# Optimization experiments

Hardware: AMD Instinct MI355X
Metric: run time of the kernel (lower is better)

The kernel has to match this reference:

```python
import jax, jax.numpy as jnp
import numpy as np

BN_EPS = 1e-5
W_SCALE = 0.05  # keep pre-softmax logits in a sane range with random weights


def setup_inputs() -> dict:
    key = jax.random.key(0)
    ks = jax.random.split(key, 8)
    b, C, H, W = 2, 512, 80, 80
    Ck, Cv, Co = 256, 256, 512
    return {
        "x": jax.random.normal(ks[0], (b, C, H, W), dtype=jnp.float32),
        "wk": jax.random.normal(ks[1], (Ck, C), dtype=jnp.float32) * W_SCALE,
        "bk": jax.random.normal(ks[2], (Ck,), dtype=jnp.float32) * W_SCALE,
        "gamma": jnp.ones((Ck,), dtype=jnp.float32),
        "beta": jnp.zeros((Ck,), dtype=jnp.float32),
        "rmean": jnp.zeros((Ck,), dtype=jnp.float32),
        "rvar": jnp.ones((Ck,), dtype=jnp.float32),
        "wv": jax.random.normal(ks[3], (Cv, C), dtype=jnp.float32) * W_SCALE,
        "bv": jax.random.normal(ks[4], (Cv,), dtype=jnp.float32) * W_SCALE,
        "wW": jax.random.normal(ks[5], (Co, Cv), dtype=jnp.float32) * W_SCALE,
        "bW": jax.random.normal(ks[6], (Co,), dtype=jnp.float32) * W_SCALE,
    }


def reference(x, wk, bk, gamma, beta, rmean, rvar, wv, bv, wW, bW):
    b, C, H, Wd = x.shape
    N = H * Wd
    Ck = wk.shape[0]
    Cv = wv.shape[0]
    # f_key == f_query (shared module): 1x1 conv + BN(inference) + ReLU
    k = jnp.einsum('bchw,oc->bohw', x, wk) + bk[:, None, None]
    scale_bn = gamma / jnp.sqrt(rvar + BN_EPS)
    k = (k - rmean[:, None, None]) * scale_bn[:, None, None] + beta[:, None, None]
    k = jax.nn.relu(k).reshape(b, Ck, N)          # [b, Ck, N]
    q = jnp.transpose(k, (0, 2, 1))               # [b, N, Ck] (query shares weights with key)
    # f_value: plain 1x1 conv
    v = (jnp.einsum('bchw,oc->bohw', x, wv) + bv[:, None, None]).reshape(b, Cv, N)
    sim = jnp.einsum('bnc,bcm->bnm', q, k) * (Ck ** -0.5)  # [b, N, N]
    sim = jax.nn.softmax(sim, axis=-1)
    ctx = jnp.einsum('bnm,bvm->bvn', sim, v).reshape(b, Cv, H, Wd)
    out = jnp.einsum('bvhw,ov->bohw', ctx, wW) + bW[:, None, None]
    return out
```

## Files before the change

kernel.cpp:

```cpp
#include <hip/hip_runtime.h>
#include <stdint.h>

typedef __attribute__((ext_vector_type(8))) short bf16x8;
typedef __attribute__((ext_vector_type(4))) float f32x4;

__device__ __forceinline__ ushort f2bf(float f) {
    union { float f; uint32_t i; } v; v.f = f;
    uint32_t r = v.i + 0x7fff + ((v.i >> 16) & 1);
    return (ushort)(r >> 16);
}
__device__ __forceinline__ uint32_t cvtpk(float lo, float hi) {
    uint32_t r;
    asm("v_cvt_pk_bf16_f32 %0, %1, %2" : "=v"(r) : "v"(lo), "v"(hi));
    return r;
}

typedef unsigned int uint_as1 __attribute__((address_space(1)));
typedef unsigned int uint_as3 __attribute__((address_space(3)));
__device__ __forceinline__ void async16(const void* g, void* l) {
    __builtin_amdgcn_global_load_lds((const uint_as1*)g, (uint_as3*)l, 16, 0, 0);
}

__global__ void prep_all(const float* __restrict__ wk, const float* __restrict__ wv,
                         const float* __restrict__ wW,
                         const float* __restrict__ bk, const float* __restrict__ gamma,
                         const float* __restrict__ beta, const float* __restrict__ rmean,
                         const float* __restrict__ rvar,
                         ushort* __restrict__ wkb, ushort* __restrict__ wvb,
                         ushort* __restrict__ wWb,
                         float* __restrict__ scaleA, float* __restrict__ shiftA) {
    const int b = blockIdx.x;
    if (b == 1536) {
        int i = threadIdx.x;
        float s = gamma[i] * rsqrtf(rvar[i] + 1e-5f);
        scaleA[i] = 0.25f * s;
        shiftA[i] = 0.25f * ((bk[i] - rmean[i]) * s + beta[i]);
        return;
    }
    const int i = (b & 511) * 256 + threadIdx.x;
    const float* src = (b < 512) ? wk : (b < 1024) ? wv : wW;
    ushort* dst = (b < 512) ? wkb : (b < 1024) ? wvb : wWb;
    dst[i] = f2bf(src[i]);
}

__global__ void transpose_cvt(const float* __restrict__ x, ushort* __restrict__ xt) {
    __shared__ float t[32][33];
    int b = blockIdx.z;
    int n0 = blockIdx.x * 32, c0 = blockIdx.y * 32;
    const float* xb = x + (size_t)b * 512 * 6400;
    ushort* xtb = xt + (size_t)b * 6400 * 512;
    int tx = threadIdx.x, ty = threadIdx.y;
    t[ty][tx] = xb[(size_t)(c0 + ty) * 6400 + n0 + tx];
    __syncthreads();
    xtb[(size_t)(n0 + ty) * 512 + c0 + tx] = f2bf(t[tx][ty]);
}

template <int EPI>
__device__ __forceinline__ void gemm_body(
    int bxi, int byi, int bzi,
    const ushort* __restrict__ A, const ushort* __restrict__ B, void* __restrict__ Cout,
    int K, int lda, int ldb, int ldc,
    size_t zsa, size_t zsb, size_t zsc,
    const float* __restrict__ vec0, const float* __restrict__ vec1,
    float* __restrict__ rsum, ushort* smem) {

    A += (size_t)bzi * zsa;
    B += (size_t)bzi * zsb;

    const int tid = threadIdx.x;
    const int lane = tid & 63, wave = tid >> 6;
    const int wm = wave & 1, wn = wave >> 1;
    const int bM = byi * 128, bN = bxi * 128;

    const int sr = lane >> 2;
    const int scs = ((lane & 3) ^ ((lane >> 3) & 3)) * 8;
    const ushort* gA0 = A + (size_t)(bM + wave * 32 + sr) * lda + scs;
    const ushort* gA1 = gA0 + (size_t)16 * lda;
    const ushort* gB0 = B + (size_t)(bN + wave * 32 + sr) * ldb + scs;
    const ushort* gB1 = gB0 + (size_t)16 * ldb;
    ushort* lAw = &smem[wave * 1024];
    ushort* lBw = &smem[3 * 4096 + wave * 1024];

    const int rowA = wm * 64;
    const int rowB = wn * 64;
    const int fr = lane & 15;
    const int fk = ((lane >> 4) ^ ((fr >> 1) & 3)) * 8;

    f32x4 acc[4][4] = {};
    const int nT = K >> 5;

    auto stage = [&](int t, int buf) {
        const int k0 = t * 32;
        const int ob = buf * 4096;
        async16(gA0 + k0, lAw + ob);
        async16(gA1 + k0, lAw + ob + 512);
        async16(gB0 + k0, lBw + ob);
        async16(gB1 + k0, lBw + ob + 512);
    };

    stage(0, 0);
    if (nT > 1) stage(1, 1);

    for (int t = 0; t < nT; ++t) {
        if (t + 1 < nT) { asm volatile("s_waitcnt vmcnt(4)" ::: "memory"); }
        else            { asm volatile("s_waitcnt vmcnt(0)" ::: "memory"); }
        __builtin_amdgcn_sched_barrier(0);
        __builtin_amdgcn_s_barrier();
        __builtin_amdgcn_sched_barrier(0);
        if (t + 2 < nT) stage(t + 2, (t + 2) % 3);
        const int cur = t % 3;
        const ushort* lA = &smem[cur * 4096];
        const ushort* lB = &smem[3 * 4096 + cur * 4096];
        bf16x8 af[4], bff[4];
#pragma unroll
        for (int mi = 0; mi < 4; mi++)
            af[mi] = *(const bf16x8*)&lA[(rowA + mi * 16 + fr) * 32 + fk];
#pragma unroll
        for (int ni = 0; ni < 4; ni++)
            bff[ni] = *(const bf16x8*)&lB[(rowB + ni * 16 + fr) * 32 + fk];
#pragma unroll
        for (int mi = 0; mi < 4; mi++)
#pragma unroll
            for (int ni = 0; ni < 4; ni++)
                acc[mi][ni] = __builtin_amdgcn_mfma_f32_16x16x32_bf16(af[mi], bff[ni], acc[mi][ni], 0, 0, 0);
        __builtin_amdgcn_sched_barrier(0);
    }
    __builtin_amdgcn_s_barrier();
    __builtin_amdgcn_sched_barrier(0);

    float* Cf = (float*)Cout + (size_t)bzi * zsc;
    ushort* Cu = (ushort*)Cout + (size_t)bzi * zsc;
    float* lt = (float*)smem;
    const int g4 = (lane >> 4) * 4;
    const int cl = lane & 15;
    const int lr = tid >> 3;
    const int ch = tid & 7;

    if (EPI == 6) {
        const bool diag = (bxi == byi);
        float creg[16];
#pragma unroll
        for (int i = 0; i < 16; i++) creg[i] = 0.f;
#pragma unroll
        for (int mi = 0; mi < 4; ++mi) {
#pragma unroll
            for (int ni = 0; ni < 4; ++ni) {
                const int lcol = wn * 64 + ni * 16 + cl;
#pragma unroll
                for (int r = 0; r < 4; ++r)
                    lt[(wm * 16 + g4 + r) * 132 + lcol] = acc[mi][ni][r];
            }
            __syncthreads();
            const int brow = (lr < 16) ? (mi * 16 + lr) : (64 + mi * 16 + (lr - 16));
            const int grow = bM + brow;
            const int gcol = bN + ch * 16;
            float vv[16];
#pragma unroll
            for (int i = 0; i < 16; i += 4) {
                f32x4 q = *(const f32x4*)&lt[lr * 132 + ch * 16 + i];
                vv[i] = __expf(q[0]); vv[i + 1] = __expf(q[1]);
                vv[i + 2] = __expf(q[2]); vv[i + 3] = __expf(q[3]);
            }
            float ssum = 0.f;
#pragma unroll
            for (int i = 0; i < 16; i++) { ssum += vv[i]; creg[i] += vv[i]; }
            ssum += __shfl_down(ssum, 4, 8);
            ssum += __shfl_down(ssum, 2, 8);
            ssum += __shfl_down(ssum, 1, 8);
            if (ch == 0) rsum[(size_t)bxi * 6400 + grow] = ssum;
            uint4 q0 = { cvtpk(vv[0], vv[1]), cvtpk(vv[2], vv[3]),
                         cvtpk(vv[4], vv[5]), cvtpk(vv[6], vv[7]) };
            uint4 q1 = { cvtpk(vv[8], vv[9]), cvtpk(vv[10], vv[11]),
                         cvtpk(vv[12], vv[13]), cvtpk(vv[14], vv[15]) };
            *(uint4*)&Cu[(size_t)grow * ldc + gcol] = q0;
            *(uint4*)&Cu[(size_t)grow * ldc + gcol + 8] = q1;
            if (!diag) {
#pragma unroll
                for (int i = 0; i < 16; i++) lt[lr * 132 + ch * 16 + i] = vv[i];
                __syncthreads();
                const int j = tid >> 1, h = tid & 1;
                ushort mo[16];
#pragma unroll
                for (int i = 0; i < 16; i += 2) {
                    float a = lt[(h * 16 + i) * 132 + j];
                    float b2 = lt[(h * 16 + i + 1) * 132 + j];
                    *(uint32_t*)&mo[i] = cvtpk(a, b2);
                }
                const size_t mbase = (size_t)(bN + j) * ldc + bM + h * 64 + mi * 16;
                *(uint4*)&Cu[mbase] = *(const uint4*)&mo[0];
                *(uint4*)&Cu[mbase + 8] = *(const uint4*)&mo[8];
            }
            __syncthreads();
        }
        if (!diag) {
#pragma unroll
            for (int i = 0; i < 16; i++) lt[lr * 132 + ch * 16 + i] = creg[i];
            __syncthreads();
            if (tid < 128) {
                float s = 0.f;
#pragma unroll
                for (int r = 0; r < 32; r++) s += lt[r * 132 + tid];
                rsum[(size_t)byi * 6400 + bN + tid] = s;
            }
        }
        return;
    }

#pragma unroll
    for (int mi = 0; mi < 4; ++mi) {
#pragma unroll
        for (int ni = 0; ni < 4; ++ni) {
            const int lcol = wn * 64 + ni * 16 + cl;
#pragma unroll
            for (int r = 0; r < 4; ++r)
                lt[(wm * 16 + g4 + r) * 132 + lcol] = acc[mi][ni][r];
        }
        __syncthreads();
        {
            const int brow = (lr < 16) ? (mi * 16 + lr) : (64 + mi * 16 + (lr - 16));
            const int grow = bM + brow;
            const int gcol = bN + ch * 16;
            float vv[16];
#pragma unroll
            for (int i = 0; i < 16; i += 4) {
                f32x4 q = *(const f32x4*)&lt[lr * 132 + ch * 16 + i];
                vv[i] = q[0]; vv[i + 1] = q[1]; vv[i + 2] = q[2]; vv[i + 3] = q[3];
            }
            if (EPI == 1) {
#pragma unroll
                for (int i = 0; i < 16; i++)
                    vv[i] = fmaxf(vv[i] * vec0[gcol + i] + vec1[gcol + i], 0.f);
            }
            if (EPI == 2 || EPI == 3) {
                const float rb = vec0[grow];
#pragma unroll
                for (int i = 0; i < 16; i++) vv[i] += rb;
            }
            if (EPI == 3 || EPI == 4) {
#pragma unroll
                for (int i = 0; i < 16; i += 4) {
                    f32x4 q = { vv[i], vv[i + 1], vv[i + 2], vv[i + 3] };
                    *(f32x4*)&Cf[(size_t)grow * ldc + gcol + i] = q;
                }
            } else {
                uint4 q0 = { cvtpk(vv[0], vv[1]), cvtpk(vv[2], vv[3]),
                             cvtpk(vv[4], vv[5]), cvtpk(vv[6], vv[7]) };
                uint4 q1 = { cvtpk(vv[8], vv[9]), cvtpk(vv[10], vv[11]),
                             cvtpk(vv[12], vv[13]), cvtpk(vv[14], vv[15]) };
                *(uint4*)&Cu[(size_t)grow * ldc + gcol] = q0;
                *(uint4*)&Cu[(size_t)grow * ldc + gcol + 8] = q1;
            }
        }
        __syncthreads();
    }
}

template <int EPI>
__global__ __launch_bounds__(256) void gemm_nt(
    const ushort* __restrict__ A, const ushort* __restrict__ B, void* __restrict__ Cout,
    int K, int lda, int ldb, int ldc,
    size_t zsa, size_t zsb, size_t zsc,
    const float* __restrict__ vec0, const float* __restrict__ vec1,
    float* __restrict__ rsum) {
    __shared__ __align__(16) ushort smem[6 * 4096];
    if (EPI == 6 && blockIdx.x < blockIdx.y) return;
    gemm_body<EPI>(blockIdx.x, blockIdx.y, blockIdx.z, A, B, Cout, K, lda, ldb, ldc,
                   zsa, zsb, zsc, vec0, vec1, rsum, smem);
}

__global__ __launch_bounds__(256) void k_kv(
    const ushort* __restrict__ Xt, const ushort* __restrict__ wkb,
    const ushort* __restrict__ wvb, ushort* __restrict__ Kt, ushort* __restrict__ V,
    const float* __restrict__ scaleA, const float* __restrict__ shiftA,
    const float* __restrict__ bv) {
    __shared__ __align__(16) ushort smem[6 * 4096];
    const int id = blockIdx.x;
    if (id < 200) {
        gemm_body<1>(id & 1, (id >> 1) % 50, id / 100, Xt, wkb, Kt,
                     512, 512, 512, 256, 3276800, 0, 1638400, scaleA, shiftA, nullptr, smem);
    } else {
        const int i = id - 200;
        gemm_body<2>(i % 50, (i / 50) % 2, i / 100, wvb, Xt, V,
                     512, 512, 512, 6400, 0, 3276800, 1638400, bv, nullptr, nullptr, smem);
    }
}

__global__ __launch_bounds__(256) void k_pv_s(
    const ushort* __restrict__ S0, const ushort* __restrict__ V0, float* __restrict__ part,
    const ushort* __restrict__ Kt1, ushort* __restrict__ S1, float* __restrict__ rowsum1) {
    __shared__ __align__(16) ushort smem[6 * 4096];
    const int id = blockIdx.x;
    if (id < 500) {
        gemm_body<4>(id & 1, (id >> 1) % 50, id / 100, S0, V0, part,
                     1280, 6400, 6400, 256, 1280, 1280, 1638400, nullptr, nullptr, nullptr, smem);
    } else {
        const int sid = id - 500;
        const int sx = sid % 50, sy = sid / 50;
        if (sx < sy) return;
        gemm_body<6>(sx, sy, 0, Kt1, Kt1, S1,
                     256, 256, 256, 6400, 0, 0, 0, nullptr, nullptr, rowsum1, smem);
    }
}

__global__ __launch_bounds__(256) void reduce_ctx(const float* __restrict__ part, ushort* __restrict__ ctx,
                                                  const float* __restrict__ rsum) {
    const size_t CH = 1638400;
    size_t i = ((size_t)blockIdx.x * 256 + threadIdx.x) * 4;
    float4 a = *(const float4*)&part[i];
#pragma unroll
    for (int c = 1; c < 5; c++) {
        float4 s = *(const float4*)&part[i + (size_t)c * CH];
        a.x += s.x; a.y += s.y; a.z += s.z; a.w += s.w;
    }
    const int row = (int)(i >> 8);
    float s = 0.f;
#pragma unroll
    for (int xb = 0; xb < 50; xb++) s += rsum[(size_t)xb * 6400 + row];
    const float w = 1.f / s;
    uint2 o = { cvtpk(a.x * w, a.y * w), cvtpk(a.z * w, a.w * w) };
    *(uint2*)&ctx[i] = o;
}

extern "C" void kernel_launch(void* const* d_in, const int* in_sizes, int n_in,
                              void* d_out, int out_size, void* d_ws, size_t ws_size,
                              hipStream_t stream) {
    (void)in_sizes; (void)n_in; (void)out_size; (void)ws_size;
    const float* x     = (const float*)d_in[0];
    const float* wk    = (const float*)d_in[1];
    const float* bk    = (const float*)d_in[2];
    const float* gamma = (const float*)d_in[3];
    const float* beta  = (const float*)d_in[4];
    const float* rmean = (const float*)d_in[5];
    const float* rvar  = (const float*)d_in[6];
    const float* wv    = (const float*)d_in[7];
    const float* bv    = (const float*)d_in[8];
    const float* wW    = (const float*)d_in[9];
    const float* bW    = (const float*)d_in[10];
    float* out = (float*)d_out;

    ushort* Xt   = (ushort*)d_ws;
    ushort* wkb  = Xt + 6553600;
    ushort* wvb  = wkb + 131072;
    ushort* wWb  = wvb + 131072;
    ushort* Kt   = wWb + 131072;
    ushort* V    = Kt + 3276800;
    ushort* ctxT = V + 3276800;
    ushort* S0   = ctxT + 3276800;
    ushort* S1   = S0 + 40960000;
    float* scaleA = (float*)(S1 + 40960000);
    float* shiftA = scaleA + 256;
    float* rowsum0 = shiftA + 256;
    float* rowsum1 = rowsum0 + 320000;
    float* part   = rowsum1 + 320000;

    prep_all<<<1537, 256, 0, stream>>>(wk, wv, wW, bk, gamma, beta, rmean, rvar,
                                       wkb, wvb, wWb, scaleA, shiftA);
    transpose_cvt<<<dim3(200, 16, 2), dim3(32, 32), 0, stream>>>(x, Xt);

    k_kv<<<400, 256, 0, stream>>>(Xt, wkb, wvb, Kt, V, scaleA, shiftA, bv);

    ushort* Kt0 = Kt;
    ushort* Kt1 = Kt + 1638400;
    ushort* V0b = V;
    ushort* V1b = V + 1638400;

    gemm_nt<6><<<dim3(50, 50), 256, 0, stream>>>(Kt0, Kt0, S0, 256, 256, 256, 6400,
                                                 0, 0, 0, nullptr, nullptr, rowsum0);

    k_pv_s<<<3000, 256, 0, stream>>>(S0, V0b, part, Kt1, S1, rowsum1);

    reduce_ctx<<<1600, 256, 0, stream>>>(part, ctxT, rowsum0);

    gemm_nt<4><<<dim3(2, 50, 5), 256, 0, stream>>>(S1, V1b, part, 1280, 6400, 6400, 256,
                                                   1280, 1280, 1638400, nullptr, nullptr, nullptr);

    reduce_ctx<<<1600, 256, 0, stream>>>(part, ctxT + 1638400, rowsum1);

    gemm_nt<3><<<dim3(50, 4, 2), 256, 0, stream>>>(wWb, ctxT, out, 256, 256, 256, 6400,
                                                   0, 1638400, 3276800, bW, nullptr, nullptr);
}
```

Before: 297.4 us.

## Batch both images per launch and double-buffer K-loop in pairs of tiles

The GEMM main loop now stages two 32-wide K tiles per barrier into four LDS buffers, which halves the number of barriers and waits but raises LDS use from 48KB to 64KB per block. The launch schedule is also restructured. The S computation for both images runs in one launch, the PV GEMM for both images runs as one launch with a 4-way K split of 1600 instead of 5 splits of 1280, and the two reduction launches are merged into one. This replaces the old overlap of PV0 with S1 and cuts the launch count. The larger shared memory footprint may lower occupancy, and vmcnt(0) waits drain all outstanding loads before each pair of tiles.

After: 291.1 us. 1.02x faster.

```diff
diff --git a/kernel.cpp b/kernel.cpp
--- a/kernel.cpp
+++ b/kernel.cpp
@@ -79,7 +79,7 @@
     const ushort* gB0 = B + (size_t)(bN + wave * 32 + sr) * ldb + scs;
     const ushort* gB1 = gB0 + (size_t)16 * ldb;
     ushort* lAw = &smem[wave * 1024];
-    ushort* lBw = &smem[3 * 4096 + wave * 1024];
+    ushort* lBw = &smem[4 * 4096 + wave * 1024];
 
     const int rowA = wm * 64;
     const int rowB = wn * 64;
@@ -88,6 +88,7 @@
 
     f32x4 acc[4][4] = {};
     const int nT = K >> 5;
+    const int nE = nT >> 1;
 
     auto stage = [&](int t, int buf) {
         const int k0 = t * 32;
@@ -99,30 +100,36 @@
     };
 
     stage(0, 0);
-    if (nT > 1) stage(1, 1);
-
-    for (int t = 0; t < nT; ++t) {
-        if (t + 1 < nT) { asm volatile("s_waitcnt vmcnt(4)" ::: "memory"); }
-        else            { asm volatile("s_waitcnt vmcnt(0)" ::: "memory"); }
+    stage(1, 1);
+
+    for (int e = 0; e < nE; ++e) {
+        asm volatile("s_waitcnt vmcnt(0)" ::: "memory");
         __builtin_amdgcn_sched_barrier(0);
         __builtin_amdgcn_s_barrier();
         __builtin_amdgcn_sched_barrier(0);
-        if (t + 2 < nT) stage(t + 2, (t + 2) % 3);
-        const int cur = t % 3;
-        const ushort* lA = &smem[cur * 4096];
-        const ushort* lB = &smem[3 * 4096 + cur * 4096];
-        bf16x8 af[4], bff[4];
-#pragma unroll
-        for (int mi = 0; mi < 4; mi++)
-            af[mi] = *(const bf16x8*)&lA[(rowA + mi * 16 + fr) * 32 + fk];
-#pragma unroll
-        for (int ni = 0; ni < 4; ni++)
-            bff[ni] = *(const bf16x8*)&lB[(rowB + ni * 16 + fr) * 32 + fk];
-#pragma unroll
-        for (int mi = 0; mi < 4; mi++)
+        if (e + 1 < nE) {
+            const int p = ((e + 1) & 1) * 2;
+            stage(2 * e + 2, p);
+            stage(2 * e + 3, p + 1);
+        }
+        const int pc = (e & 1) * 2;
+#pragma unroll
+        for (int h = 0; h < 2; ++h) {
+            const ushort* lA = &smem[(pc + h) * 4096];
+            const ushort* lB = &smem[4 * 4096 + (pc + h) * 4096];
+            bf16x8 af[4], bff[4];
+#pragma unroll
+            for (int mi = 0; mi < 4; mi++)
+                af[mi] = *(const bf16x8*)&lA[(rowA + mi * 16 + fr) * 32 + fk];
 #pragma unroll
             for (int ni = 0; ni < 4; ni++)
-                acc[mi][ni] = __builtin_amdgcn_mfma_f32_16x16x32_bf16(af[mi], bff[ni], acc[mi][ni], 0, 0, 0);
+                bff[ni] = *(const bf16x8*)&lB[(rowB + ni * 16 + fr) * 32 + fk];
+#pragma unroll
+            for (int mi = 0; mi < 4; mi++)
+#pragma unroll
+                for (int ni = 0; ni < 4; ni++)
+                    acc[mi][ni] = __builtin_amdgcn_mfma_f32_16x16x32_bf16(af[mi], bff[ni], acc[mi][ni], 0, 0, 0);
+        }
         __builtin_amdgcn_sched_barrier(0);
     }
     __builtin_amdgcn_s_barrier();
@@ -262,8 +269,7 @@
     size_t zsa, size_t zsb, size_t zsc,
     const float* __restrict__ vec0, const float* __restrict__ vec1,
     float* __restrict__ rsum) {
-    __shared__ __align__(16) ushort smem[6 * 4096];
-    if (EPI == 6 && blockIdx.x < blockIdx.y) return;
+    __shared__ __align__(16) ushort smem[8 * 4096];
     gemm_body<EPI>(blockIdx.x, blockIdx.y, blockIdx.z, A, B, Cout, K, lda, ldb, ldc,
                    zsa, zsb, zsc, vec0, vec1, rsum, smem);
 }
@@ -273,7 +279,7 @@
     const ushort* __restrict__ wvb, ushort* __restrict__ Kt, ushort* __restrict__ V,
     const float* __restrict__ scaleA, const float* __restrict__ shiftA,
     const float* __restrict__ bv) {
-    __shared__ __align__(16) ushort smem[6 * 4096];
+    __shared__ __align__(16) ushort smem[8 * 4096];
     const int id = blockIdx.x;
     if (id < 200) {
         gemm_body<1>(id & 1, (id >> 1) % 50, id / 100, Xt, wkb, Kt,
@@ -285,40 +291,53 @@
     }
 }
 
-__global__ __launch_bounds__(256) void k_pv_s(
-    const ushort* __restrict__ S0, const ushort* __restrict__ V0, float* __restrict__ part,
-    const ushort* __restrict__ Kt1, ushort* __restrict__ S1, float* __restrict__ rowsum1) {
-    __shared__ __align__(16) ushort smem[6 * 4096];
+__global__ __launch_bounds__(256) void k_s_both(
+    const ushort* __restrict__ Kt, ushort* __restrict__ S0, float* __restrict__ rowsum) {
+    __shared__ __align__(16) ushort smem[8 * 4096];
+    if (blockIdx.x < blockIdx.y) return;
+    const int z = blockIdx.z;
+    const ushort* K = Kt + (size_t)z * 1638400;
+    ushort* S = S0 + (size_t)z * 40960000;
+    float* rs = rowsum + (size_t)z * 320000;
+    gemm_body<6>(blockIdx.x, blockIdx.y, 0, K, K, S,
+                 256, 256, 256, 6400, 0, 0, 0, nullptr, nullptr, rs, smem);
+}
+
+__global__ __launch_bounds__(256) void k_pv_both(
+    const ushort* __restrict__ S0, const ushort* __restrict__ V, float* __restrict__ part) {
+    __shared__ __align__(16) ushort smem[8 * 4096];
+    const int z = blockIdx.z;
+    const int b = z >> 2, c = z & 3;
+    const ushort* A = S0 + (size_t)b * 40960000 + (size_t)c * 1600;
+    const ushort* B = V + (size_t)b * 1638400 + (size_t)c * 1600;
+    float* C = part + (size_t)b * 6553600 + (size_t)c * 1638400;
+    gemm_body<4>(blockIdx.x, blockIdx.y, 0, A, B, C,
+                 1600, 6400, 6400, 256, 0, 0, 0, nullptr, nullptr, nullptr, smem);
+}
+
+__global__ __launch_bounds__(256) void reduce_both(const float* __restrict__ part,
+                                                   ushort* __restrict__ ctx,
+                                                   const float* __restrict__ rowsum) {
     const int id = blockIdx.x;
-    if (id < 500) {
-        gemm_body<4>(id & 1, (id >> 1) % 50, id / 100, S0, V0, part,
-                     1280, 6400, 6400, 256, 1280, 1280, 1638400, nullptr, nullptr, nullptr, smem);
-    } else {
-        const int sid = id - 500;
-        const int sx = sid % 50, sy = sid / 50;
-        if (sx < sy) return;
-        gemm_body<6>(sx, sy, 0, Kt1, Kt1, S1,
-                     256, 256, 256, 6400, 0, 0, 0, nullptr, nullptr, rowsum1, smem);
-    }
-}
-
-__global__ __launch_bounds__(256) void reduce_ctx(const float* __restrict__ part, ushort* __restrict__ ctx,
-                                                  const float* __restrict__ rsum) {
-    const size_t CH = 1638400;
-    size_t i = ((size_t)blockIdx.x * 256 + threadIdx.x) * 4;
-    float4 a = *(const float4*)&part[i];
-#pragma unroll
-    for (int c = 1; c < 5; c++) {
-        float4 s = *(const float4*)&part[i + (size_t)c * CH];
+    const int b = id >= 1600;
+    const int lid = id - b * 1600;
+    const float* p = part + (size_t)b * 6553600;
+    const float* rs = rowsum + (size_t)b * 320000;
+    ushort* cx = ctx + (size_t)b * 1638400;
+    size_t i = ((size_t)lid * 256 + threadIdx.x) * 4;
+    float4 a = *(const float4*)&p[i];
+#pragma unroll
+    for (int c = 1; c < 4; c++) {
+        float4 s = *(const float4*)&p[i + (size_t)c * 1638400];
         a.x += s.x; a.y += s.y; a.z += s.z; a.w += s.w;
     }
     const int row = (int)(i >> 8);
     float s = 0.f;
 #pragma unroll
-    for (int xb = 0; xb < 50; xb++) s += rsum[(size_t)xb * 6400 + row];
+    for (int xb = 0; xb < 50; xb++) s += rs[(size_t)xb * 6400 + row];
     const float w = 1.f / s;
     uint2 o = { cvtpk(a.x * w, a.y * w), cvtpk(a.z * w, a.w * w) };
-    *(uint2*)&ctx[i] = o;
+    *(uint2*)&cx[i] = o;
 }
 
 extern "C" void kernel_launch(void* const* d_in, const int* in_sizes, int n_in,
@@ -346,12 +365,10 @@
     ushort* V    = Kt + 3276800;
     ushort* ctxT = V + 3276800;
     ushort* S0   = ctxT + 3276800;
-    ushort* S1   = S0 + 40960000;
-    float* scaleA = (float*)(S1 + 40960000);
+    float* scaleA = (float*)(S0 + 2 * 40960000);
     float* shiftA = scaleA + 256;
-    float* rowsum0 = shiftA + 256;
-    float* rowsum1 = rowsum0 + 320000;
-    float* part   = rowsum1 + 320000;
+    float* rowsum = shiftA + 256;
+    float* part   = rowsum + 640000;
 
     prep_all<<<1537, 256, 0, stream>>>(wk, wv, wW, bk, gamma, beta, rmean, rvar,
                                        wkb, wvb, wWb, scaleA, shiftA);
@@ -359,22 +376,11 @@
 
     k_kv<<<400, 256, 0, stream>>>(Xt, wkb, wvb, Kt, V, scaleA, shiftA, bv);
 
-    ushort* Kt0 = Kt;
-    ushort* Kt1 = Kt + 1638400;
-    ushort* V0b = V;
-    ushort* V1b = V + 1638400;
-
-    gemm_nt<6><<<dim3(50, 50), 256, 0, stream>>>(Kt0, Kt0, S0, 256, 256, 256, 6400,
-                                                 0, 0, 0, nullptr, nullptr, rowsum0);
-
-    k_pv_s<<<3000, 256, 0, stream>>>(S0, V0b, part, Kt1, S1, rowsum1);
-
-    reduce_ctx<<<1600, 256, 0, stream>>>(part, ctxT, rowsum0);
-
-    gemm_nt<4><<<dim3(2, 50, 5), 256, 0, stream>>>(S1, V1b, part, 1280, 6400, 6400, 256,
-                                                   1280, 1280, 1638400, nullptr, nullptr, nullptr);
-
-    reduce_ctx<<<1600, 256, 0, stream>>>(part, ctxT + 1638400, rowsum1);
+    k_s_both<<<dim3(50, 50, 2), 256, 0, stream>>>(Kt, S0, rowsum);
+
+    k_pv_both<<<dim3(2, 50, 8), 256, 0, stream>>>(S0, V, part);
+
+    reduce_both<<<3200, 256, 0, stream>>>(part, ctxT, rowsum);
 
     gemm_nt<3><<<dim3(50, 4, 2), 256, 0, stream>>>(wWb, ctxT, out, 256, 256, 256, 6400,
                                                    0, 1638400, 3276800, bW, nullptr, nullptr);
```
